# Optimization experiments

Hardware: AMD Instinct MI355X
Metric: run time of the kernel (lower is better)

## Reference

```python
import jax, jax.numpy as jnp
import numpy as np

HID, H, D, DFF = 128, 4, 128, 2048   # hidden_dim, nheads, out_feats per head, dim_feedforward
N, E, B = 32768, 524288, 32
EPS = 1e-5
SLOPE = 0.2  # DGL EdgeGATConv negative_slope default


def setup_inputs() -> dict:
    key = jax.random.key(0)
    ks = jax.random.split(key, 16)
    s = 0.05
    return {
        "h": jax.random.normal(ks[0], (N, HID), jnp.float32),
        "e": jax.random.normal(ks[1], (E, 1), jnp.float32),
        "src": jax.random.randint(ks[2], (E,), 0, N, jnp.int32),
        "dst": jax.random.randint(ks[3], (E,), 0, N, jnp.int32),
        "batch_size": B,
        # EdgeGATConv params (fc / fc_edge / res_fc are bias-free in DGL)
        "W_fc": jax.random.normal(ks[4], (HID, H * D), jnp.float32) * s,
        "attn_l": jax.random.normal(ks[5], (H, D), jnp.float32) * s,
        "attn_r": jax.random.normal(ks[6], (H, D), jnp.float32) * s,
        "W_fe": jax.random.normal(ks[7], (1, H * D), jnp.float32) * s,
        "attn_e": jax.random.normal(ks[8], (H, D), jnp.float32) * s,
        "W_res": jax.random.normal(ks[9], (HID, H * D), jnp.float32) * s,
        "gat_bias": jnp.zeros((H * D,), jnp.float32),
        # linear_mha + norms + FFN
        "W_mha": jax.random.normal(ks[10], (H * D, HID), jnp.float32) * s,
        "b_mha": jnp.zeros((HID,), jnp.float32),
        "n1_g": jnp.ones((HID,), jnp.float32),
        "n1_b": jnp.zeros((HID,), jnp.float32),
        "n2_g": jnp.ones((HID,), jnp.float32),
        "n2_b": jnp.zeros((HID,), jnp.float32),
        "W1": jax.random.normal(ks[11], (HID, DFF), jnp.float32) * s,
        "b1": jnp.zeros((DFF,), jnp.float32),
        "W2": jax.random.normal(ks[12], (DFF, HID), jnp.float32) * s,
        "b2": jnp.zeros((HID,), jnp.float32),
    }


def _ln(x, g, b):
    mu = x.mean(-1, keepdims=True)
    var = ((x - mu) ** 2).mean(-1, keepdims=True)
    return (x - mu) * jax.lax.rsqrt(var + EPS) * g + b


def reference(h, e, src, dst, batch_size, W_fc, attn_l, attn_r, W_fe, attn_e,
              W_res, gat_bias, W_mha, b_mha, n1_g, n1_b, n2_g, n2_b,
              W1, b1, W2, b2):
    n = h.shape[0]
    h0 = h
    # --- EdgeGATConv (eval mode: dropouts are identity) ---
    ft = (h @ W_fc).reshape(n, H, D)                         # (N,H,D)
    el = jnp.einsum("nhd,hd->nh", ft, attn_l)                # (N,H)
    er = jnp.einsum("nhd,hd->nh", ft, attn_r)
    fe = (e @ W_fe).reshape(-1, H, D)                        # (E,H,D)
    ee = jnp.einsum("ehd,hd->eh", fe, attn_e)                # (E,H)
    sc = jax.nn.leaky_relu(el[src] + er[dst] + ee, SLOPE)    # (E,H)
    # segment softmax over incoming edges of each dst node
    m = jax.ops.segment_max(sc, dst, num_segments=n)         # (N,H)
    m = jnp.where(jnp.isfinite(m), m, 0.0)                   # empty segments
    w = jnp.exp(sc - m[dst])
    z = jax.ops.segment_sum(w, dst, num_segments=n)
    zd = z[dst]
    alpha = w / jnp.where(zd == 0, 1.0, zd)                  # (E,H)
    msg = ft[src] * alpha[:, :, None]                        # (E,H,D)
    rst = jax.ops.segment_sum(msg, dst, num_segments=n)      # (N,H,D)
    rst = rst + (h0 @ W_res).reshape(n, H, D) + gat_bias.reshape(1, H, D)
    # --- transformer wrapper ---
    x = jax.nn.relu(rst).reshape(n, H * D)
    x = jax.nn.relu(x @ W_mha + b_mha)
    x = _ln(h0 + x, n1_g, n1_b)
    x = x.reshape(batch_size, -1, x.shape[1])                # (B, N/B, HID)
    ff = jax.nn.relu(x @ W1 + b1) @ W2 + b2
    return _ln(x + ff, n2_g, n2_b)
```

## Files before the change

kernel.cpp:

```cpp
#include <hip/hip_runtime.h>
#include <hip/hip_bf16.h>
#include <hip/hip_fp16.h>

#define N_NODES 32768
#define E_EDGES 524288
#define HIDDIM 128
#define FDIM 512
#define DFF 2048
#define LN_EPS 1e-5f
#define SLOPE 0.2f
#define CAP 64

typedef __bf16 bf16_t;
typedef __bf16 bf16x8 __attribute__((ext_vector_type(8)));
typedef float f32x4 __attribute__((ext_vector_type(4)));
typedef float f32x2 __attribute__((ext_vector_type(2)));

#define GLD_LDS16(gp, lp) __builtin_amdgcn_global_load_lds( \
    (const __attribute__((address_space(1))) unsigned int*)(gp), \
    (__attribute__((address_space(3))) unsigned int*)(lp), 16, 0, 0)

__device__ inline unsigned char f32_to_e4m3(float v) {
#if __has_builtin(__builtin_amdgcn_cvt_pk_fp8_f32)
    return (unsigned char)(__builtin_amdgcn_cvt_pk_fp8_f32(v, v, 0, false) & 0xff);
#else
    unsigned bits = __float_as_uint(v);
    unsigned sign = (bits >> 24) & 0x80;
    float av = fabsf(v);
    if (av >= 448.f) return (unsigned char)(sign | 0x7E);
    int e = (int)((bits >> 23) & 0xFF) - 127;
    if (e < -6) { int n = (int)rintf(av * 512.f); return (unsigned char)(sign | n); }
    float ulp = exp2f((float)(e - 3));
    int n = (int)rintf(av / ulp);
    if (n == 16) { e += 1; n = 8; }
    return (unsigned char)(sign | ((e + 7) << 3) | (n - 8));
#endif
}
template<bool HI>
__device__ inline f32x2 e4m3x2_to_f32(unsigned u) {
#if __has_builtin(__builtin_amdgcn_cvt_pk_f32_fp8)
    return __builtin_amdgcn_cvt_pk_f32_fp8(u, HI);
#else
    f32x2 r;
    unsigned b0 = HI ? ((u >> 16) & 0xff) : (u & 0xff);
    unsigned b1 = HI ? ((u >> 24) & 0xff) : ((u >> 8) & 0xff);
    unsigned bs[2] = {b0, b1};
    for (int i = 0; i < 2; ++i) {
        unsigned b = bs[i];
        float s = (b & 0x80) ? -1.f : 1.f;
        int e = (b >> 3) & 15, m = b & 7;
        float v = e ? (8 + m) * exp2f((float)(e - 10)) : m * exp2f(-9.f);
        r[i] = s * v;
    }
    return r;
#endif
}

__device__ inline void pack_range(const float* __restrict__ B, bf16_t* __restrict__ out,
                                  int id, int N) {
    const int g = id / N, n = id % N;
    union { bf16_t b[8]; uint4 u; } pk;
#pragma unroll
    for (int j = 0; j < 8; ++j) pk.b[j] = (bf16_t)B[(size_t)(g * 8 + j) * N + n];
    *(uint4*)(out + (size_t)id * 8) = pk.u;
}

__global__ __launch_bounds__(256) void prep_kernel(const float* __restrict__ h, bf16_t* __restrict__ hb,
                                                   const float* __restrict__ W_fc, bf16_t* __restrict__ Wfc_p,
                                                   const float* __restrict__ W_res, bf16_t* __restrict__ Wres_p,
                                                   const float* __restrict__ W_mha, bf16_t* __restrict__ Wmha_p,
                                                   const float* __restrict__ W1, bf16_t* __restrict__ W1_p,
                                                   const float* __restrict__ W2, bf16_t* __restrict__ W2_p,
                                                   const float* __restrict__ W_fe, const float* __restrict__ attn_e,
                                                   float* __restrict__ ce) {
    int bid = blockIdx.x;
    const int tid = threadIdx.x;
    if (bid < 4096) {
        const int id = bid * 256 + tid;
        const float4 v = ((const float4*)h)[id];
        union { bf16_t b[4]; uint2 u; } pk;
        pk.b[0] = (bf16_t)v.x; pk.b[1] = (bf16_t)v.y; pk.b[2] = (bf16_t)v.z; pk.b[3] = (bf16_t)v.w;
        *(uint2*)(hb + (size_t)id * 4) = pk.u;
        return;
    }
    bid -= 4096;
    if (bid < 32)  { pack_range(W_fc,  Wfc_p,  bid * 256 + tid, 512);  return; }
    bid -= 32;
    if (bid < 32)  { pack_range(W_res, Wres_p, bid * 256 + tid, 512);  return; }
    bid -= 32;
    if (bid < 32)  { pack_range(W_mha, Wmha_p, bid * 256 + tid, 128);  return; }
    bid -= 32;
    if (bid < 128) { pack_range(W1,    W1_p,   bid * 256 + tid, 2048); return; }
    bid -= 128;
    if (bid < 128) { pack_range(W2,    W2_p,   bid * 256 + tid, 128);  return; }
    if (tid < 128) {
        const float4 w = ((const float4*)W_fe)[tid];
        const float4 a = ((const float4*)attn_e)[tid];
        float p = w.x * a.x + w.y * a.y + w.z * a.z + w.w * a.w;
        for (int off = 16; off; off >>= 1) p += __shfl_down(p, off, 32);
        if ((tid & 31) == 0) ce[tid >> 5] = p;
    }
}

__global__ __launch_bounds__(256, 2) void gemm_ftres(const bf16_t* __restrict__ A,
                                                     const bf16_t* __restrict__ Bf,
                                                     const bf16_t* __restrict__ Brs,
                                                     const float* __restrict__ attn_l,
                                                     const float* __restrict__ attn_r,
                                                     unsigned char* __restrict__ ft8,
                                                     float* __restrict__ el,
                                                     float* __restrict__ er,
                                                     bf16_t* __restrict__ res) {
    __shared__ __align__(16) bf16_t lA[4096];
    __shared__ __align__(16) bf16_t lBf[4096];
    __shared__ __align__(16) bf16_t lBr[4096];
    __shared__ float s_el[2][128], s_er[2][128];
    const int tid = threadIdx.x, lane = tid & 63, wave = tid >> 6;
    const int wm = (wave >> 1) * 64, wn = (wave & 1) * 64;
    const int row0 = blockIdx.y * 128;
    const int head = blockIdx.x, col0 = head * 128;
    const int ko = lane >> 4, rl = lane & 15;
    f32x4 accf[4][4] = {};
    f32x4 accr[4][4] = {};
    const int c0 = tid, c1 = tid + 256;
    const int g0 = c0 >> 7, m0 = c0 & 127;
    const int g1 = c1 >> 7, m1 = c1 & 127;
    for (int k0 = 0; k0 < 128; k0 += 32) {
        __syncthreads();
        GLD_LDS16(A + (size_t)(row0 + m0) * 128 + k0 + g0 * 8, lA + c0 * 8);
        GLD_LDS16(A + (size_t)(row0 + m1) * 128 + k0 + g1 * 8, lA + c1 * 8);
        GLD_LDS16(Bf + ((size_t)(k0 / 8 + g0) * 512 + col0 + m0) * 8, lBf + c0 * 8);
        GLD_LDS16(Bf + ((size_t)(k0 / 8 + g1) * 512 + col0 + m1) * 8, lBf + c1 * 8);
        GLD_LDS16(Brs + ((size_t)(k0 / 8 + g0) * 512 + col0 + m0) * 8, lBr + c0 * 8);
        GLD_LDS16(Brs + ((size_t)(k0 / 8 + g1) * 512 + col0 + m1) * 8, lBr + c1 * 8);
        __syncthreads();
        bf16x8 af[4], bff[4], bfr[4];
#pragma unroll
        for (int i = 0; i < 4; ++i) {
            af[i]  = *(const bf16x8*)&lA[(ko * 128 + wm + i * 16 + rl) * 8];
            bff[i] = *(const bf16x8*)&lBf[(ko * 128 + wn + i * 16 + rl) * 8];
            bfr[i] = *(const bf16x8*)&lBr[(ko * 128 + wn + i * 16 + rl) * 8];
        }
#pragma unroll
        for (int i = 0; i < 4; ++i)
#pragma unroll
            for (int j = 0; j < 4; ++j) {
                accf[i][j] = __builtin_amdgcn_mfma_f32_16x16x32_bf16(af[i], bff[j], accf[i][j], 0, 0, 0);
                accr[i][j] = __builtin_amdgcn_mfma_f32_16x16x32_bf16(af[i], bfr[j], accr[i][j], 0, 0, 0);
            }
    }
    const int cr = (lane >> 4) * 4, cc = lane & 15;
    float al[4], ar[4];
#pragma unroll
    for (int j = 0; j < 4; ++j) {
        al[j] = attn_l[col0 + wn + j * 16 + cc];
        ar[j] = attn_r[col0 + wn + j * 16 + cc];
    }
#pragma unroll
    for (int i = 0; i < 4; ++i)
#pragma unroll
        for (int r = 0; r < 4; ++r) {
            const int row = row0 + wm + i * 16 + cr + r;
            float pel = 0.f, per = 0.f;
#pragma unroll
            for (int j = 0; j < 4; ++j) {
                const int col = col0 + wn + j * 16 + cc;
                const float v = accf[i][j][r];
                ft8[(size_t)row * 512 + col] = f32_to_e4m3(v);
                res[(size_t)row * 512 + col] = (bf16_t)accr[i][j][r];
                pel += v * al[j];
                per += v * ar[j];
            }
#pragma unroll
            for (int m = 1; m < 16; m <<= 1) {
                pel += __shfl_xor(pel, m);
                per += __shfl_xor(per, m);
            }
            if (cc == 0) {
                s_el[wn >> 6][wm + i * 16 + cr + r] = pel;
                s_er[wn >> 6][wm + i * 16 + cr + r] = per;
            }
        }
    __syncthreads();
    if (tid < 128) {
        el[(size_t)(row0 + tid) * 4 + head] = s_el[0][tid] + s_el[1][tid];
        er[(size_t)(row0 + tid) * 4 + head] = s_er[0][tid] + s_er[1][tid];
    }
}

__global__ __launch_bounds__(256) void gemm_mha_ln(const bf16_t* __restrict__ A,
                                                   const bf16_t* __restrict__ Bp,
                                                   const float* __restrict__ bias,
                                                   const float* __restrict__ h0,
                                                   const float* __restrict__ gamma,
                                                   const float* __restrict__ beta,
                                                   bf16_t* __restrict__ out) {
    __shared__ __align__(16) bf16_t lA[1024];
    __shared__ __align__(16) bf16_t lB[4096];
    __shared__ float s_s1[4][32], s_s2[4][32], s_mu[32], s_rs[32];
    const int tid = threadIdx.x, lane = tid & 63, wave = tid >> 6;
    const int wn = wave * 32;
    const int row0 = blockIdx.x * 32;
    const int ko = lane >> 4, rl = lane & 15;
    f32x4 acc[2][2] = {};
    for (int k0 = 0; k0 < 512; k0 += 32) {
        __syncthreads();
        if (tid < 128) {
            const int g = tid >> 5, m = tid & 31;
            GLD_LDS16(A + (size_t)(row0 + m) * 512 + k0 + g * 8, lA + tid * 8);
        }
        {
            const int g0 = tid >> 7, n0 = tid & 127;
            GLD_LDS16(Bp + ((size_t)(k0 / 8 + g0) * 128 + n0) * 8, lB + tid * 8);
            const int c1 = tid + 256, g1 = c1 >> 7, n1 = c1 & 127;
            GLD_LDS16(Bp + ((size_t)(k0 / 8 + g1) * 128 + n1) * 8, lB + c1 * 8);
        }
        __syncthreads();
        bf16x8 af[2], bfr[2];
#pragma unroll
        for (int i = 0; i < 2; ++i)
            af[i] = *(const bf16x8*)&lA[(ko * 32 + i * 16 + rl) * 8];
#pragma unroll
        for (int j = 0; j < 2; ++j)
            bfr[j] = *(const bf16x8*)&lB[(ko * 128 + wn + j * 16 + rl) * 8];
#pragma unroll
        for (int i = 0; i < 2; ++i)
#pragma unroll
            for (int j = 0; j < 2; ++j)
                acc[i][j] = __builtin_amdgcn_mfma_f32_16x16x32_bf16(af[i], bfr[j], acc[i][j], 0, 0, 0);
    }
    const int cr = (lane >> 4) * 4, cc = lane & 15;
#pragma unroll
    for (int j = 0; j < 2; ++j) {
        const int col = wn + j * 16 + cc;
        const float bb = bias[col];
#pragma unroll
        for (int i = 0; i < 2; ++i)
#pragma unroll
            for (int r = 0; r < 4; ++r) {
                const int row = row0 + i * 16 + cr + r;
                acc[i][j][r] = fmaxf(acc[i][j][r] + bb, 0.f) + h0[(size_t)row * 128 + col];
            }
    }
#pragma unroll
    for (int i = 0; i < 2; ++i)
#pragma unroll
        for (int r = 0; r < 4; ++r) {
            float s1 = 0.f, s2 = 0.f;
#pragma unroll
            for (int j = 0; j < 2; ++j) { const float v = acc[i][j][r]; s1 += v; s2 += v * v; }
#pragma unroll
            for (int m = 1; m < 16; m <<= 1) {
                s1 += __shfl_xor(s1, m);
                s2 += __shfl_xor(s2, m);
            }
            if (cc == 0) {
                s_s1[wave][i * 16 + cr + r] = s1;
                s_s2[wave][i * 16 + cr + r] = s2;
            }
        }
    __syncthreads();
    if (tid < 32) {
        const float a = s_s1[0][tid] + s_s1[1][tid] + s_s1[2][tid] + s_s1[3][tid];
        const float q = s_s2[0][tid] + s_s2[1][tid] + s_s2[2][tid] + s_s2[3][tid];
        const float mu = a * (1.f / 128.f);
        s_mu[tid] = mu;
        s_rs[tid] = rsqrtf(q * (1.f / 128.f) - mu * mu + LN_EPS);
    }
    __syncthreads();
#pragma unroll
    for (int j = 0; j < 2; ++j) {
        const int col = wn + j * 16 + cc;
        const float gg = gamma[col], bb = beta[col];
#pragma unroll
        for (int i = 0; i < 2; ++i)
#pragma unroll
            for (int r = 0; r < 4; ++r) {
                const int rloc = i * 16 + cr + r;
                out[(size_t)(row0 + rloc) * 128 + col] =
                    (bf16_t)((acc[i][j][r] - s_mu[rloc]) * s_rs[rloc] * gg + bb);
            }
    }
}

__global__ __launch_bounds__(512, 2) void ffn_fused(const bf16_t* __restrict__ x3,
                                                    const bf16_t* __restrict__ W1p,
                                                    const float* __restrict__ b1,
                                                    const bf16_t* __restrict__ W2p,
                                                    const float* __restrict__ b2,
                                                    const float* __restrict__ gamma,
                                                    const float* __restrict__ beta,
                                                    float* __restrict__ out) {
    __shared__ __align__(16) bf16_t lW1[3][8192];
    __shared__ __align__(16) bf16_t lW2[4][8192];
    __shared__ __align__(16) bf16_t lY[2][8192];
    __shared__ float s_s1[2][128], s_s2[2][128], s_mu[128], s_rs[128];
    const int tid = threadIdx.x, lane = tid & 63, wave = tid >> 6;
    const int kh  = wave & 1;
    const int ds  = wave & 3;
    const int cg  = (wave >> 1) & 1;
    const int rg  = wave >> 2;
    const int wr  = rg * 64;
    const int wc1 = ds * 16;
    const int wc2 = cg * 64;
    const int row0 = blockIdx.x * 128;
    const int ko = lane >> 4, rl = lane & 15;
    const int cr = ko * 4, cc = rl;

    bf16_t* lX = &lW1[0][0];
#pragma unroll
    for (int it = 0; it < 4; ++it) {
        const int c = it * 512 + tid, g = c >> 7, m = c & 127;
        GLD_LDS16(x3 + (size_t)(row0 + m) * 128 + g * 8, lX + c * 8);
    }
    __syncthreads();
    bf16x8 afx[4][4];
#pragma unroll
    for (int ir = 0; ir < 4; ++ir)
#pragma unroll
        for (int kk = 0; kk < 4; ++kk)
            afx[ir][kk] = *(const bf16x8*)&lX[((kk * 4 + ko) * 128 + wr + ir * 16 + rl) * 8];
    asm volatile("s_waitcnt lgkmcnt(0)" ::: "memory");
    __builtin_amdgcn_s_barrier();
    __builtin_amdgcn_sched_barrier(0);

    auto stage_chunk = [&](int chn, bf16_t* w1d, bf16_t* w2d) {
#pragma unroll
        for (int it = 0; it < 2; ++it) {
            const int c = it * 512 + tid, g = c >> 6, n = c & 63;
            GLD_LDS16(W1p + ((size_t)g * 2048 + chn * 64 + n) * 8, w1d + c * 8);
        }
#pragma unroll
        for (int it = 0; it < 2; ++it) {
            const int c = it * 512 + tid, g = c >> 7, n = c & 127;
            GLD_LDS16(W2p + ((size_t)(chn * 8 + g) * 128 + n) * 8, w2d + c * 8);
        }
    };

    f32x4 xacc[4][4] = {};

    auto gemm1 = [&](int chn, const bf16_t* w1c, bf16_t* ydst) {
        f32x4 yacc[4] = {};
        __builtin_amdgcn_s_setprio(1);
#pragma unroll
        for (int kk = 0; kk < 4; ++kk) {
            const bf16x8 bw = *(const bf16x8*)&w1c[((kk * 4 + ko) * 64 + wc1 + rl) * 8];
#pragma unroll
            for (int ir = 0; ir < 4; ++ir)
                yacc[ir] = __builtin_amdgcn_mfma_f32_16x16x32_bf16(bw, afx[ir][kk], yacc[ir], 0, 0, 0);
        }
        __builtin_amdgcn_s_setprio(0);
        const int dffb = wc1 + cr;
        const float4 bb = *(const float4*)(b1 + chn * 64 + dffb);
#pragma unroll
        for (int ir = 0; ir < 4; ++ir) {
            const int rowx = wr + ir * 16 + cc;
            union { bf16_t b[4]; uint2 u; } pk;
            pk.b[0] = (bf16_t)fmaxf(yacc[ir][0] + bb.x, 0.f);
            pk.b[1] = (bf16_t)fmaxf(yacc[ir][1] + bb.y, 0.f);
            pk.b[2] = (bf16_t)fmaxf(yacc[ir][2] + bb.z, 0.f);
            pk.b[3] = (bf16_t)fmaxf(yacc[ir][3] + bb.w, 0.f);
            *(uint2*)&ydst[((dffb >> 3) * 128 + rowx) * 8 + (dffb & 7)] = pk.u;
        }
    };

    auto gemm2 = [&](const bf16_t* w2c, const bf16_t* ysrc) {
        bf16x8 ay[4], bw2[4];
#pragma unroll
        for (int ir = 0; ir < 4; ++ir)
            ay[ir] = *(const bf16x8*)&ysrc[((kh * 4 + ko) * 128 + wr + ir * 16 + rl) * 8];
#pragma unroll
        for (int j = 0; j < 4; ++j)
            bw2[j] = *(const bf16x8*)&w2c[((kh * 4 + ko) * 128 + wc2 + j * 16 + rl) * 8];
        __builtin_amdgcn_s_setprio(1);
#pragma unroll
        for (int ir = 0; ir < 4; ++ir)
#pragma unroll
            for (int j = 0; j < 4; ++j)
                xacc[ir][j] = __builtin_amdgcn_mfma_f32_16x16x32_bf16(ay[ir], bw2[j], xacc[ir][j], 0, 0, 0);
        __builtin_amdgcn_s_setprio(0);
    };

#pragma unroll
    for (int pc = 0; pc < 2; ++pc)
        stage_chunk(pc, lW1[pc], lW2[pc]);
    asm volatile("s_waitcnt vmcnt(4)" ::: "memory");
    __builtin_amdgcn_s_barrier();
    __builtin_amdgcn_sched_barrier(0);

    stage_chunk(2, lW1[2], lW2[2]);
    gemm1(0, lW1[0], lY[0]);
    __builtin_amdgcn_sched_barrier(0);
    asm volatile("s_waitcnt vmcnt(4) lgkmcnt(0)" ::: "memory");
    __builtin_amdgcn_s_barrier();
    __builtin_amdgcn_sched_barrier(0);

    int r1 = 1, sb1 = 0, r2 = 0, sb2 = 3, p = 1;
#pragma unroll 1
    for (int i = 1; i < 32; ++i) {
        if (i < 30)
            stage_chunk(i + 2, lW1[sb1], lW2[sb2]);
        gemm1(i, lW1[r1], lY[p]);
        gemm2(lW2[r2], lY[p ^ 1]);
        __builtin_amdgcn_sched_barrier(0);
        if (i < 30)
            asm volatile("s_waitcnt vmcnt(4) lgkmcnt(0)" ::: "memory");
        else if (i == 30)
            asm volatile("s_waitcnt vmcnt(2) lgkmcnt(0)" ::: "memory");
        else
            asm volatile("s_waitcnt vmcnt(0) lgkmcnt(0)" ::: "memory");
        __builtin_amdgcn_s_barrier();
        __builtin_amdgcn_sched_barrier(0);
        r1 = (r1 == 2) ? 0 : r1 + 1;
        sb1 = (sb1 == 2) ? 0 : sb1 + 1;
        r2 = (r2 == 3) ? 0 : r2 + 1;
        sb2 = (sb2 == 3) ? 0 : sb2 + 1;
        p ^= 1;
    }
    gemm2(lW2[3], lY[1]);

    __syncthreads();
    {
        const int q = (wave >> 1) & 3;
        float* scr = (q < 2) ? ((float*)&lW1[0][0] + q * 4352)
                             : ((float*)&lW2[0][0] + (q - 2) * 4352);
        if (kh) {
#pragma unroll
            for (int ir = 0; ir < 4; ++ir)
#pragma unroll
                for (int j = 0; j < 4; ++j)
                    *(f32x4*)(scr + lane * 68 + (ir * 4 + j) * 4) = xacc[ir][j];
        }
        __syncthreads();
        if (!kh) {
#pragma unroll
            for (int ir = 0; ir < 4; ++ir)
#pragma unroll
                for (int j = 0; j < 4; ++j)
                    xacc[ir][j] += *(const f32x4*)(scr + lane * 68 + (ir * 4 + j) * 4);
        }
    }

    if (!kh) {
#pragma unroll
        for (int j = 0; j < 4; ++j) {
            const int col = wc2 + j * 16 + cc;
            const float bb = b2[col];
#pragma unroll
            for (int ir = 0; ir < 4; ++ir)
#pragma unroll
                for (int r = 0; r < 4; ++r) {
                    const int row = wr + ir * 16 + cr + r;
                    xacc[ir][j][r] += bb + (float)x3[(size_t)(row0 + row) * 128 + col];
                }
        }
#pragma unroll
        for (int ir = 0; ir < 4; ++ir)
#pragma unroll
            for (int r = 0; r < 4; ++r) {
                float s1v = 0.f, s2v = 0.f;
#pragma unroll
                for (int j = 0; j < 4; ++j) { const float v = xacc[ir][j][r]; s1v += v; s2v += v * v; }
#pragma unroll
                for (int m = 1; m < 16; m <<= 1) {
                    s1v += __shfl_xor(s1v, m);
                    s2v += __shfl_xor(s2v, m);
                }
                if (cc == 0) {
                    s_s1[cg][wr + ir * 16 + cr + r] = s1v;
                    s_s2[cg][wr + ir * 16 + cr + r] = s2v;
                }
            }
    }
    __syncthreads();
    if (tid < 128) {
        const float a = s_s1[0][tid] + s_s1[1][tid];
        const float q = s_s2[0][tid] + s_s2[1][tid];
        const float mu = a * (1.f / 128.f);
        s_mu[tid] = mu;
        s_rs[tid] = rsqrtf(q * (1.f / 128.f) - mu * mu + LN_EPS);
    }
    __syncthreads();
    if (!kh) {
#pragma unroll
        for (int j = 0; j < 4; ++j) {
            const int col = wc2 + j * 16 + cc;
            const float gg = gamma[col], bb = beta[col];
#pragma unroll
            for (int ir = 0; ir < 4; ++ir)
#pragma unroll
                for (int r = 0; r < 4; ++r) {
                    const int rloc = wr + ir * 16 + cr + r;
                    out[(size_t)(row0 + rloc) * 128 + col] =
                        (xacc[ir][j][r] - s_mu[rloc]) * s_rs[rloc] * gg + bb;
                }
        }
    }
}

__global__ __launch_bounds__(256) void edge_build(const float* __restrict__ evals,
                                                  const int* __restrict__ src,
                                                  const int* __restrict__ dst,
                                                  const float* __restrict__ el,
                                                  const float* __restrict__ er,
                                                  const float* __restrict__ ce,
                                                  int* __restrict__ cursor,
                                                  uint4* __restrict__ csr) {
    const int e = blockIdx.x * 256 + threadIdx.x;
    const int s = src[e], d = dst[e];
    const float ev = evals[e];
    const float4 l = *(const float4*)(el + (size_t)s * 4);
    const float4 r = *(const float4*)(er + (size_t)d * 4);
    const float4 c = *(const float4*)ce;
    float4 w;
    {
        float v;
        v = l.x + r.x + ev * c.x; v = v >= 0.f ? v : SLOPE * v; w.x = __expf(v);
        v = l.y + r.y + ev * c.y; v = v >= 0.f ? v : SLOPE * v; w.y = __expf(v);
        v = l.z + r.z + ev * c.z; v = v >= 0.f ? v : SLOPE * v; w.z = __expf(v);
        v = l.w + r.w + ev * c.w; v = v >= 0.f ? v : SLOPE * v; w.w = __expf(v);
    }
    const int pos = atomicAdd(&cursor[d], 1);
    if (pos < CAP) {
        uint4 rec;
        rec.x = (unsigned)__half_as_ushort(__float2half(w.x)) |
                ((unsigned)__half_as_ushort(__float2half(w.y)) << 16);
        rec.y = (unsigned)__half_as_ushort(__float2half(w.z)) |
                ((unsigned)__half_as_ushort(__float2half(w.w)) << 16);
        rec.z = (unsigned)s;
        rec.w = 0u;
        csr[(size_t)d * CAP + pos] = rec;
    }
}

__device__ inline float w_of(const uint4& rec, int ht) {
    const unsigned pair = (ht < 2) ? rec.x : rec.y;
    const unsigned sh = (ht & 1) ? (pair >> 16) : (pair & 0xffffu);
    return __half2float(__ushort_as_half((unsigned short)sh));
}

__global__ __launch_bounds__(128) void aggregate_kernel(const unsigned char* __restrict__ ft8,
                                                        const bf16_t* __restrict__ res,
                                                        const int* __restrict__ cursor,
                                                        const uint4* __restrict__ csr,
                                                        const float* __restrict__ gat_bias,
                                                        bf16_t* __restrict__ x1) {
    const int n = blockIdx.x, t = threadIdx.x;
    __shared__ uint4 s_rec[CAP];
    const int deg = min(cursor[n], CAP);
    const int ht = t >> 5;
    if (t < deg) s_rec[t] = csr[(size_t)n * CAP + t];
    __syncthreads();
    float4 acc = {0.f, 0.f, 0.f, 0.f};
    float z = 0.f;
    int j = 0;
    for (; j + 8 <= deg; j += 8) {
        unsigned u[8];
        float w[8];
#pragma unroll
        for (int q = 0; q < 8; ++q) {
            const uint4 rc = s_rec[j + q];
            w[q] = w_of(rc, ht);
            u[q] = *(const unsigned*)(ft8 + (size_t)rc.z * 512 + t * 4);
        }
#pragma unroll
        for (int q = 0; q < 8; ++q) {
            z += w[q];
            const f32x2 lo = e4m3x2_to_f32<false>(u[q]), hi = e4m3x2_to_f32<true>(u[q]);
            acc.x += w[q] * lo[0]; acc.y += w[q] * lo[1];
            acc.z += w[q] * hi[0]; acc.w += w[q] * hi[1];
        }
    }
    for (; j < deg; ++j) {
        const uint4 rc = s_rec[j];
        const float w = w_of(rc, ht);
        z += w;
        const unsigned u = *(const unsigned*)(ft8 + (size_t)rc.z * 512 + t * 4);
        const f32x2 lo = e4m3x2_to_f32<false>(u);
        const f32x2 hi = e4m3x2_to_f32<true>(u);
        acc.x += w * lo[0]; acc.y += w * lo[1];
        acc.z += w * hi[0]; acc.w += w * hi[1];
    }
    const float rz = deg > 0 ? 1.f / z : 0.f;
    const uint2 ur = *(const uint2*)(res + (size_t)n * FDIM + t * 4);
    const float4 gb = ((const float4*)gat_bias)[t];
    union { bf16_t b[4]; uint2 u; } pk;
    pk.b[0] = (bf16_t)fmaxf(acc.x * rz + __uint_as_float(ur.x << 16) + gb.x, 0.f);
    pk.b[1] = (bf16_t)fmaxf(acc.y * rz + __uint_as_float(ur.x & 0xFFFF0000u) + gb.y, 0.f);
    pk.b[2] = (bf16_t)fmaxf(acc.z * rz + __uint_as_float(ur.y << 16) + gb.z, 0.f);
    pk.b[3] = (bf16_t)fmaxf(acc.w * rz + __uint_as_float(ur.y & 0xFFFF0000u) + gb.w, 0.f);
    *(uint2*)(x1 + (size_t)n * FDIM + t * 4) = pk.u;
}

extern "C" void kernel_launch(void* const* d_in, const int* in_sizes, int n_in,
                              void* d_out, int out_size, void* d_ws, size_t ws_size,
                              hipStream_t stream) {
    const float* h        = (const float*)d_in[0];
    const float* evals    = (const float*)d_in[1];
    const int*   src      = (const int*)d_in[2];
    const int*   dst      = (const int*)d_in[3];
    const float* W_fc     = (const float*)d_in[5];
    const float* attn_l   = (const float*)d_in[6];
    const float* attn_r   = (const float*)d_in[7];
    const float* W_fe     = (const float*)d_in[8];
    const float* attn_e   = (const float*)d_in[9];
    const float* W_res    = (const float*)d_in[10];
    const float* gat_bias = (const float*)d_in[11];
    const float* W_mha    = (const float*)d_in[12];
    const float* b_mha    = (const float*)d_in[13];
    const float* n1_g     = (const float*)d_in[14];
    const float* n1_b     = (const float*)d_in[15];
    const float* n2_g     = (const float*)d_in[16];
    const float* n2_b     = (const float*)d_in[17];
    const float* W1       = (const float*)d_in[18];
    const float* b1       = (const float*)d_in[19];
    const float* W2       = (const float*)d_in[20];
    const float* b2       = (const float*)d_in[21];

    char* ws = (char*)d_ws;
    unsigned char* ft8 = (unsigned char*)(ws + 0);
    bf16_t* res     = (bf16_t*)(ws + 16777216ull);
    bf16_t* x1      = (bf16_t*)(ws + 50331648ull);
    uint4*  csr     = (uint4*) (ws + 83886080ull);
    bf16_t* x3b     = (bf16_t*)(ws + 125829120ull);
    bf16_t* hb      = (bf16_t*)(ws + 134217728ull);
    bf16_t* Wfc_p   = (bf16_t*)(ws + 142606336ull);
    bf16_t* Wres_p  = (bf16_t*)(ws + 142737408ull);
    bf16_t* Wmha_p  = (bf16_t*)(ws + 142868480ull);
    bf16_t* W1_p    = (bf16_t*)(ws + 142999552ull);
    bf16_t* W2_p    = (bf16_t*)(ws + 143523840ull);
    float*  el      = (float*) (ws + 144048128ull);
    float*  er      = (float*) (ws + 144572416ull);
    float*  ce      = (float*) (ws + 145096704ull);
    int*    cursor  = (int*)   (ws + 145096768ull);

    if (ws_size < 146000000ull) return;

    (void)hipMemsetAsync(cursor, 0, 131072, stream);

    prep_kernel<<<4449, 256, 0, stream>>>(h, hb, W_fc, Wfc_p, W_res, Wres_p,
                                          W_mha, Wmha_p, W1, W1_p, W2, W2_p,
                                          W_fe, attn_e, ce);
    gemm_ftres<<<dim3(4, 256), 256, 0, stream>>>(hb, Wfc_p, Wres_p, attn_l, attn_r, ft8, el, er, res);
    edge_build<<<E_EDGES / 256, 256, 0, stream>>>(evals, src, dst, el, er, ce, cursor, csr);
    aggregate_kernel<<<N_NODES, 128, 0, stream>>>(ft8, res, cursor, csr, gat_bias, x1);
    gemm_mha_ln<<<1024, 256, 0, stream>>>(x1, Wmha_p, b_mha, h, n1_g, n1_b, x3b);
    ffn_fused<<<256, 512, 0, stream>>>(x3b, W1_p, b1, W2_p, b2, n2_g, n2_b, (float*)d_out);
}
```

Before: 282.5 us.

## Fuse MHA projection and first LayerNorm into the FFN kernel

Merges gemm_mha_ln into the FFN kernel so each 128-row block first computes x1@W_mha, bias, ReLU, residual and LayerNorm, then writes the normalized tile straight into LDS as the FFN input. This removes one kernel launch and the global round trip that reloaded x3 for the FFN, although x3 is still stashed to global for the residual read. The cost is that the MHA GEMM now runs on only 256 blocks instead of 1024, with a small synchronous K loop and no load pipelining, which may leave it underutilising the GPU.

New measurement: 283.2 us. Within noise of the previous version (+0.3%).

```diff
diff --git a/kernel.cpp b/kernel.cpp
--- a/kernel.cpp
+++ b/kernel.cpp
@@ -188,109 +188,20 @@
     }
 }
 
-__global__ __launch_bounds__(256) void gemm_mha_ln(const bf16_t* __restrict__ A,
-                                                   const bf16_t* __restrict__ Bp,
-                                                   const float* __restrict__ bias,
+__global__ __launch_bounds__(512, 2) void ffn_mega(const bf16_t* __restrict__ x1,
+                                                   const bf16_t* __restrict__ Wm,
+                                                   const float* __restrict__ b_mha,
                                                    const float* __restrict__ h0,
+                                                   const float* __restrict__ n1g,
+                                                   const float* __restrict__ n1b,
+                                                   bf16_t* __restrict__ x3stash,
+                                                   const bf16_t* __restrict__ W1p,
+                                                   const float* __restrict__ b1,
+                                                   const bf16_t* __restrict__ W2p,
+                                                   const float* __restrict__ b2,
                                                    const float* __restrict__ gamma,
                                                    const float* __restrict__ beta,
-                                                   bf16_t* __restrict__ out) {
-    __shared__ __align__(16) bf16_t lA[1024];
-    __shared__ __align__(16) bf16_t lB[4096];
-    __shared__ float s_s1[4][32], s_s2[4][32], s_mu[32], s_rs[32];
-    const int tid = threadIdx.x, lane = tid & 63, wave = tid >> 6;
-    const int wn = wave * 32;
-    const int row0 = blockIdx.x * 32;
-    const int ko = lane >> 4, rl = lane & 15;
-    f32x4 acc[2][2] = {};
-    for (int k0 = 0; k0 < 512; k0 += 32) {
-        __syncthreads();
-        if (tid < 128) {
-            const int g = tid >> 5, m = tid & 31;
-            GLD_LDS16(A + (size_t)(row0 + m) * 512 + k0 + g * 8, lA + tid * 8);
-        }
-        {
-            const int g0 = tid >> 7, n0 = tid & 127;
-            GLD_LDS16(Bp + ((size_t)(k0 / 8 + g0) * 128 + n0) * 8, lB + tid * 8);
-            const int c1 = tid + 256, g1 = c1 >> 7, n1 = c1 & 127;
-            GLD_LDS16(Bp + ((size_t)(k0 / 8 + g1) * 128 + n1) * 8, lB + c1 * 8);
-        }
-        __syncthreads();
-        bf16x8 af[2], bfr[2];
-#pragma unroll
-        for (int i = 0; i < 2; ++i)
-            af[i] = *(const bf16x8*)&lA[(ko * 32 + i * 16 + rl) * 8];
-#pragma unroll
-        for (int j = 0; j < 2; ++j)
-            bfr[j] = *(const bf16x8*)&lB[(ko * 128 + wn + j * 16 + rl) * 8];
-#pragma unroll
-        for (int i = 0; i < 2; ++i)
-#pragma unroll
-            for (int j = 0; j < 2; ++j)
-                acc[i][j] = __builtin_amdgcn_mfma_f32_16x16x32_bf16(af[i], bfr[j], acc[i][j], 0, 0, 0);
-    }
-    const int cr = (lane >> 4) * 4, cc = lane & 15;
-#pragma unroll
-    for (int j = 0; j < 2; ++j) {
-        const int col = wn + j * 16 + cc;
-        const float bb = bias[col];
-#pragma unroll
-        for (int i = 0; i < 2; ++i)
-#pragma unroll
-            for (int r = 0; r < 4; ++r) {
-                const int row = row0 + i * 16 + cr + r;
-                acc[i][j][r] = fmaxf(acc[i][j][r] + bb, 0.f) + h0[(size_t)row * 128 + col];
-            }
-    }
-#pragma unroll
-    for (int i = 0; i < 2; ++i)
-#pragma unroll
-        for (int r = 0; r < 4; ++r) {
-            float s1 = 0.f, s2 = 0.f;
-#pragma unroll
-            for (int j = 0; j < 2; ++j) { const float v = acc[i][j][r]; s1 += v; s2 += v * v; }
-#pragma unroll
-            for (int m = 1; m < 16; m <<= 1) {
-                s1 += __shfl_xor(s1, m);
-                s2 += __shfl_xor(s2, m);
-            }
-            if (cc == 0) {
-                s_s1[wave][i * 16 + cr + r] = s1;
-                s_s2[wave][i * 16 + cr + r] = s2;
-            }
-        }
-    __syncthreads();
-    if (tid < 32) {
-        const float a = s_s1[0][tid] + s_s1[1][tid] + s_s1[2][tid] + s_s1[3][tid];
-        const float q = s_s2[0][tid] + s_s2[1][tid] + s_s2[2][tid] + s_s2[3][tid];
-        const float mu = a * (1.f / 128.f);
-        s_mu[tid] = mu;
-        s_rs[tid] = rsqrtf(q * (1.f / 128.f) - mu * mu + LN_EPS);
-    }
-    __syncthreads();
-#pragma unroll
-    for (int j = 0; j < 2; ++j) {
-        const int col = wn + j * 16 + cc;
-        const float gg = gamma[col], bb = beta[col];
-#pragma unroll
-        for (int i = 0; i < 2; ++i)
-#pragma unroll
-            for (int r = 0; r < 4; ++r) {
-                const int rloc = i * 16 + cr + r;
-                out[(size_t)(row0 + rloc) * 128 + col] =
-                    (bf16_t)((acc[i][j][r] - s_mu[rloc]) * s_rs[rloc] * gg + bb);
-            }
-    }
-}
-
-__global__ __launch_bounds__(512, 2) void ffn_fused(const bf16_t* __restrict__ x3,
-                                                    const bf16_t* __restrict__ W1p,
-                                                    const float* __restrict__ b1,
-                                                    const bf16_t* __restrict__ W2p,
-                                                    const float* __restrict__ b2,
-                                                    const float* __restrict__ gamma,
-                                                    const float* __restrict__ beta,
-                                                    float* __restrict__ out) {
+                                                   float* __restrict__ out) {
     __shared__ __align__(16) bf16_t lW1[3][8192];
     __shared__ __align__(16) bf16_t lW2[4][8192];
     __shared__ __align__(16) bf16_t lY[2][8192];
@@ -307,13 +218,90 @@
     const int ko = lane >> 4, rl = lane & 15;
     const int cr = ko * 4, cc = rl;
 
+    {
+        const int rg2 = wave >> 1;
+        const int cg2 = wave & 1;
+        bf16_t* lA = &lY[0][0];
+        bf16_t* lB = &lY[0][4096];
+        f32x4 am[2][4] = {};
+        for (int k0 = 0; k0 < 512; k0 += 32) {
+            __syncthreads();
+            {
+                const int g = tid >> 7, m = tid & 127;
+                GLD_LDS16(x1 + (size_t)(row0 + m) * 512 + k0 + g * 8, lA + tid * 8);
+                GLD_LDS16(Wm + ((size_t)(k0 / 8 + g) * 128 + m) * 8, lB + tid * 8);
+            }
+            __syncthreads();
+            bf16x8 af[2], bf[4];
+#pragma unroll
+            for (int i = 0; i < 2; ++i)
+                af[i] = *(const bf16x8*)&lA[(ko * 128 + rg2 * 32 + i * 16 + rl) * 8];
+#pragma unroll
+            for (int j = 0; j < 4; ++j)
+                bf[j] = *(const bf16x8*)&lB[(ko * 128 + cg2 * 64 + j * 16 + rl) * 8];
+#pragma unroll
+            for (int i = 0; i < 2; ++i)
+#pragma unroll
+                for (int j = 0; j < 4; ++j)
+                    am[i][j] = __builtin_amdgcn_mfma_f32_16x16x32_bf16(af[i], bf[j], am[i][j], 0, 0, 0);
+        }
+#pragma unroll
+        for (int j = 0; j < 4; ++j) {
+            const int col = cg2 * 64 + j * 16 + cc;
+            const float bb = b_mha[col];
+#pragma unroll
+            for (int i = 0; i < 2; ++i)
+#pragma unroll
+                for (int r = 0; r < 4; ++r) {
+                    const int row = row0 + rg2 * 32 + i * 16 + cr + r;
+                    am[i][j][r] = fmaxf(am[i][j][r] + bb, 0.f) + h0[(size_t)row * 128 + col];
+                }
+        }
+#pragma unroll
+        for (int i = 0; i < 2; ++i)
+#pragma unroll
+            for (int r = 0; r < 4; ++r) {
+                float s1 = 0.f, s2 = 0.f;
+#pragma unroll
+                for (int j = 0; j < 4; ++j) { const float v = am[i][j][r]; s1 += v; s2 += v * v; }
+#pragma unroll
+                for (int m = 1; m < 16; m <<= 1) {
+                    s1 += __shfl_xor(s1, m);
+                    s2 += __shfl_xor(s2, m);
+                }
+                if (cc == 0) {
+                    s_s1[cg2][rg2 * 32 + i * 16 + cr + r] = s1;
+                    s_s2[cg2][rg2 * 32 + i * 16 + cr + r] = s2;
+                }
+            }
+        __syncthreads();
+        if (tid < 128) {
+            const float a = s_s1[0][tid] + s_s1[1][tid];
+            const float q = s_s2[0][tid] + s_s2[1][tid];
+            const float mu = a * (1.f / 128.f);
+            s_mu[tid] = mu;
+            s_rs[tid] = rsqrtf(q * (1.f / 128.f) - mu * mu + LN_EPS);
+        }
+        __syncthreads();
+        bf16_t* lX0 = &lW1[0][0];
+#pragma unroll
+        for (int j = 0; j < 4; ++j) {
+            const int col = cg2 * 64 + j * 16 + cc;
+            const float gg = n1g[col], bbta = n1b[col];
+#pragma unroll
+            for (int i = 0; i < 2; ++i)
+#pragma unroll
+                for (int r = 0; r < 4; ++r) {
+                    const int rloc = rg2 * 32 + i * 16 + cr + r;
+                    const bf16_t v = (bf16_t)((am[i][j][r] - s_mu[rloc]) * s_rs[rloc] * gg + bbta);
+                    lX0[((col >> 3) * 128 + rloc) * 8 + (col & 7)] = v;
+                    x3stash[(size_t)(row0 + rloc) * 128 + col] = v;
+                }
+        }
+    }
+    __syncthreads();
+
     bf16_t* lX = &lW1[0][0];
-#pragma unroll
-    for (int it = 0; it < 4; ++it) {
-        const int c = it * 512 + tid, g = c >> 7, m = c & 127;
-        GLD_LDS16(x3 + (size_t)(row0 + m) * 128 + g * 8, lX + c * 8);
-    }
-    __syncthreads();
     bf16x8 afx[4][4];
 #pragma unroll
     for (int ir = 0; ir < 4; ++ir)
@@ -451,7 +439,7 @@
 #pragma unroll
                 for (int r = 0; r < 4; ++r) {
                     const int row = wr + ir * 16 + cr + r;
-                    xacc[ir][j][r] += bb + (float)x3[(size_t)(row0 + row) * 128 + col];
+                    xacc[ir][j][r] += bb + (float)x3stash[(size_t)(row0 + row) * 128 + col];
                 }
         }
 #pragma unroll
@@ -644,6 +632,6 @@
     gemm_ftres<<<dim3(4, 256), 256, 0, stream>>>(hb, Wfc_p, Wres_p, attn_l, attn_r, ft8, el, er, res);
     edge_build<<<E_EDGES / 256, 256, 0, stream>>>(evals, src, dst, el, er, ce, cursor, csr);
     aggregate_kernel<<<N_NODES, 128, 0, stream>>>(ft8, res, cursor, csr, gat_bias, x1);
-    gemm_mha_ln<<<1024, 256, 0, stream>>>(x1, Wmha_p, b_mha, h, n1_g, n1_b, x3b);
-    ffn_fused<<<256, 512, 0, stream>>>(x3b, W1_p, b1, W2_p, b2, n2_g, n2_b, (float*)d_out);
-}
+    ffn_mega<<<256, 512, 0, stream>>>(x1, Wmha_p, b_mha, h, n1_g, n1_b, x3b,
+                                      W1_p, b1, W2_p, b2, n2_g, n2_b, (float*)d_out);
+}
```
